# Kernel optimization log

Measured on AMD Instinct MI355X. Metric: run time of the kernel, lower is better.

The kernel has to match this reference:

```python
import jax, jax.numpy as jnp
import numpy as np

B, S, D = 8, 4096, 192
MEM_READ, MEM_WRITE, MEM_READY = 156, 157, 158


def setup_inputs() -> dict:
    key = jax.random.key(0)
    ks = jax.random.split(key, 9)
    inp = {"x": jax.random.normal(ks[0], (B, S, D), dtype=jnp.float32)}
    names = ["Wq_r", "Wk_r", "Wv_r", "Wo_r", "Wq_w", "Wk_w", "Wv_w", "Wo_w"]
    for i, n in enumerate(names):
        inp[n] = jax.random.normal(ks[i + 1], (D, D), dtype=jnp.float32) * 0.02
    return inp


def _attention(x, Wq, Wk, Wv, Wo):
    # single-head, non-causal PureAttention: q/k/v = x @ W.T, softmax(qk^T/sqrt(D)) v, then W_o
    q = jnp.einsum('bsd,ed->bse', x, Wq)
    k = jnp.einsum('bsd,ed->bse', x, Wk)
    v = jnp.einsum('bsd,ed->bse', x, Wv)
    scale = jnp.asarray(1.0 / np.sqrt(D), x.dtype)
    scores = jnp.einsum('bqe,bke->bqk', q, k) * scale  # [B,S,S]
    attn = jax.nn.softmax(scores, axis=-1)
    o = jnp.einsum('bqk,bke->bqe', attn, v)
    return jnp.einsum('bse,oe->bso', o, Wo)


def reference(x, Wq_r, Wk_r, Wv_r, Wo_r, Wq_w, Wk_w, Wv_w, Wo_w):
    read_flag = x[:, 0, MEM_READ]    # [B]
    write_flag = x[:, 0, MEM_WRITE]  # [B]
    read_res = _attention(x, Wq_r, Wk_r, Wv_r, Wo_r)
    write_res = _attention(x, Wq_w, Wk_w, Wv_w, Wo_w)
    rg = read_flag[:, None, None]
    wg = write_flag[:, None, None]
    out = x + rg * (read_res - x) + wg * (write_res - x)
    out = out.at[:, :, MEM_READ].set(0.0)
    out = out.at[:, :, MEM_WRITE].set(0.0)
    ready = (read_flag + write_flag)[:, None]  # broadcast over seq
    out = out.at[:, :, MEM_READY].set(jnp.broadcast_to(ready, out.shape[:2]))
    return out
```

## Files before the change

### kernel.cpp

```cpp
#include <hip/hip_runtime.h>
#include <stdint.h>

#define B_ 8
#define S_ 4096
#define D_ 192
#define M_ (B_*S_)

typedef short v8s __attribute__((ext_vector_type(8)));
typedef float v4f __attribute__((ext_vector_type(4)));
typedef unsigned short v4us __attribute__((ext_vector_type(4)));
typedef unsigned long long ull;

static __device__ __forceinline__ unsigned short f2bf(float f){
  union{float f; unsigned u;} v; v.f=f;
  unsigned u = v.u;
  unsigned r = (u + 0x7fffu + ((u>>16)&1u))>>16;
  return (unsigned short)r;
}
static __device__ __forceinline__ float fexp2(float x){
  return __builtin_amdgcn_exp2f(x);
}
static __device__ __forceinline__ unsigned cvtpk(float lo, float hi){
  unsigned r;
  asm("v_cvt_pk_bf16_f32 %0, %1, %2" : "=v"(r) : "v"(lo), "v"(hi));
  return r;
}

static __device__ __forceinline__ unsigned sw_fp8(float x){
  union{float f; unsigned u;} v; v.f = x;
  unsigned s = (v.u >> 24) & 0x80u;
  float a = fabsf(x);
  if (a < 0.001953125f) return s;
  if (a >= 240.f) return s | 0x7Eu;
  if (a < 0.015625f) {
    int m = (int)(a*512.f + 0.5f); if(m>7) m=7;
    return s | (unsigned)m;
  }
  int e = (int)((v.u >> 23) & 0xff) - 127;
  unsigned mant = (v.u >> 20) & 0x7u;
  unsigned rest = v.u & 0xFFFFFu;
  if (rest > 0x80000u || (rest == 0x80000u && (mant&1u))) mant++;
  unsigned ee = (unsigned)(e + 7);
  if (mant == 8u){ mant = 0u; ee++; }
  return s | (ee<<3) | mant;
}
template<bool HI>
static __device__ __forceinline__ unsigned pk8(float a, float b, unsigned old){
#if __has_builtin(__builtin_amdgcn_cvt_pk_fp8_f32)
  return __builtin_amdgcn_cvt_pk_fp8_f32(a, b, old, HI);
#else
  unsigned p = sw_fp8(a) | (sw_fp8(b)<<8);
  return HI ? ((old & 0x0000FFFFu) | (p<<16)) : ((old & 0xFFFF0000u) | p);
#endif
}

typedef const __attribute__((address_space(1))) unsigned int gu32;
typedef __attribute__((address_space(3))) unsigned int lu32;
#define GLL16(gp, lp) __builtin_amdgcn_global_load_lds((gu32*)(gp), (lu32*)(lp), 16, 0, 0)

__global__ void cvt_w_kernel(const float* w0,const float* w1,const float* w2,const float* w3,
                             const float* w4,const float* w5,const float* w6,const float* w7,
                             unsigned short* dst){
  int w = blockIdx.y;
  const float* src;
  switch(w){
    case 0: src=w0; break; case 1: src=w1; break; case 2: src=w2; break; case 3: src=w3; break;
    case 4: src=w4; break; case 5: src=w5; break; case 6: src=w6; break; default: src=w7; break;
  }
  int i = blockIdx.x*256 + threadIdx.x;
  float v = src[i];
  if(w==0 || w==4 || w==1 || w==5) v *= 0.32267249f;
  dst[(size_t)w*36864 + i] = f2bf(v);
}

__global__ __launch_bounds__(256) void proj_kernel(
    const float* __restrict__ x, const unsigned short* __restrict__ Wb,
    unsigned char* __restrict__ QK8, unsigned short* __restrict__ V16)
{
  __shared__ __align__(16) unsigned short Vstage[192*72];
  const size_t MDB = (size_t)M_*D_;
  const size_t MD  = (size_t)M_*D_;
  int path = blockIdx.y;
  int tid = threadIdx.x;
  int wid = tid>>6, lane = tid&63;
  int lr = lane&15, lg = lane>>4, kb = lg*8;
  int m0 = blockIdx.x*64 + wid*16;
  int row = m0 + lr;

  v8s a[6];
  #pragma unroll
  for(int c=0;c<6;c++){
    const float* xp = &x[(size_t)row*D_ + c*32 + kb];
    float4 f0 = *(const float4*)xp;
    float4 f1 = *(const float4*)(xp+4);
    v8s t;
    t[0]=(short)f2bf(f0.x); t[1]=(short)f2bf(f0.y); t[2]=(short)f2bf(f0.z); t[3]=(short)f2bf(f0.w);
    t[4]=(short)f2bf(f1.x); t[5]=(short)f2bf(f1.y); t[6]=(short)f2bf(f1.z); t[7]=(short)f2bf(f1.w);
    a[c]=t;
  }
  int bidx = m0 / S_;
  int sb   = (blockIdx.x*64) % S_;
  int sloc = wid*16 + lg*4;

  unsigned char* dstQ8 = QK8 + (size_t)path*2*MDB;
  for(int which=0; which<2; which++){
    const unsigned short* W = Wb + (size_t)(path*4 + which)*36864;
    unsigned char* dst = which==0 ? dstQ8 : dstQ8 + MDB;
    #pragma unroll
    for(int nt=0; nt<12; nt++){
      v4f acc = {0.f,0.f,0.f,0.f};
      int n = nt*16 + lr;
      #pragma unroll
      for(int c=0;c<6;c++){
        v8s bfr = *(const v8s*)&W[(size_t)n*D_ + c*32 + kb];
        acc = __builtin_amdgcn_mfma_f32_16x16x32_bf16(a[c], bfr, acc, 0,0,0);
      }
      int col = nt*16 + lr;
      int r0 = m0 + lg*4;
      #pragma unroll
      for(int r=0;r<4;r++){
        unsigned p = pk8<false>(acc[r], 0.f, 0u);
        dst[(size_t)(r0+r)*D_ + col] = (unsigned char)(p & 0xFF);
      }
    }
  }
  {
    const unsigned short* W = Wb + (size_t)(path*4 + 2)*36864;
    #pragma unroll
    for(int nt=0; nt<12; nt++){
      v4f acc = {0.f,0.f,0.f,0.f};
      int n = nt*16 + lr;
      #pragma unroll
      for(int c=0;c<6;c++){
        v8s bfr = *(const v8s*)&W[(size_t)n*D_ + c*32 + kb];
        acc = __builtin_amdgcn_mfma_f32_16x16x32_bf16(a[c], bfr, acc, 0,0,0);
      }
      int col = nt*16 + lr;
      v4us pk;
      pk[0]=f2bf(acc[0]); pk[1]=f2bf(acc[1]); pk[2]=f2bf(acc[2]); pk[3]=f2bf(acc[3]);
      *(v4us*)&Vstage[col*72 + sloc] = pk;
    }
    __syncthreads();
    unsigned short* dstV = V16 + (size_t)path*MD;
    size_t vg = (size_t)bidx*D_*S_ + sb;
    #pragma unroll
    for(int j=0;j<6;j++){
      int i = tid + j*256;
      int d = i>>3, s8 = (i&7)*8;
      *(v8s*)&dstV[vg + (size_t)d*S_ + s8] = *(const v8s*)&Vstage[d*72 + s8];
    }
  }
}

#define KSTR8 200

__global__ __launch_bounds__(512,4) void attn_kernel(
    const unsigned char* __restrict__ QK8,
    const unsigned short* __restrict__ V16,
    unsigned short* __restrict__ Ob)
{
  __shared__ __align__(16) unsigned char  KL[2][32*KSTR8];
  __shared__ __align__(16) unsigned short VL[3][192*32];

  int flat = blockIdx.x + 32*blockIdx.y + 256*blockIdx.z;
  int w = (flat&7)*64 + (flat>>3);
  int qi = w & 31;
  int b  = (w>>5) & 7;
  int z  = w>>8;

  const size_t MDB = (size_t)M_*D_;
  const unsigned char* Q8 = QK8 + (size_t)z*2*MDB;
  const unsigned char* K8 = Q8 + MDB;
  const unsigned short* Vt = V16 + (size_t)z*MDB;
  unsigned short* O = Ob + (size_t)z*MDB;

  int q0 = qi*128;
  int tid = threadIdx.x, wid=tid>>6, lane=tid&63;
  int lr = lane&15, lg = lane>>4;
  size_t bK = (size_t)b*S_*D_;
  size_t bV = (size_t)b*D_*S_;
  int qrow0 = q0 + wid*16;

  bool isK = wid < 4;
  int kt256 = tid & 255;
  int ksR = kt256>>3, ksC = (kt256&7)*24;
  int kLds = ksR*KSTR8 + ksC;
  int voff[3], vLds[3];
  #pragma unroll
  for(int j=0;j<3;j++){
    int i = (tid & 255) + j*256;
    int vrow = i>>2, vin = (i&3)*16;
    voff[j] = vrow*4096 + ((vin ^ (((vrow>>1)&3)<<4))>>1);
    vLds[j] = i*16;
  }
  int vro = ((lg*16) ^ (((lr>>1)&3)<<4)) >> 1;

  long qf8[6];
  {
    const unsigned char* qp = Q8 + bK + (size_t)(qrow0 + lr)*D_;
    #pragma unroll
    for(int c=0;c<6;c++) qf8[c] = *(const long*)(qp + c*32 + lg*8);
  }
  float lsum = 0.f;
  v4f oacc[12];
  #pragma unroll
  for(int e=0;e<12;e++) oacc[e] = (v4f){0.f,0.f,0.f,0.f};

  ull k0, k1, k2;
  auto kissue = [&](int t){
    if(isK){
      const unsigned char* kg = K8 + bK + (size_t)t*6144 + ksR*192 + ksC;
      k0 = *(const ull*)(kg);
      k1 = *(const ull*)(kg+8);
      k2 = *(const ull*)(kg+16);
    }
  };
  auto kwrite = [&](int buf){
    if(isK){
      unsigned char* d = &KL[buf][kLds];
      *(ull*)(d)    = k0;
      *(ull*)(d+8)  = k1;
      *(ull*)(d+16) = k2;
    }
  };
  auto vissue = [&](int t, int buf){
    if(!isK){
      const unsigned short* vg = Vt + bV + (size_t)t*32;
      #pragma unroll
      for(int j=0;j<3;j++) GLL16(vg + voff[j], ((unsigned char*)&VL[buf][0]) + vLds[j]);
    }
  };
  auto do_qk = [&](int kcur, v4f sacc[2]){
    __builtin_amdgcn_s_setprio(1);
    #pragma unroll
    for(int ct=0; ct<2; ct++){
      v4f s = {0.f,0.f,0.f,0.f};
      const unsigned char* rb = &KL[kcur][(ct*16+lr)*KSTR8];
      #pragma unroll
      for(int c=0;c<6;c++){
        long kf8 = *(const long*)(rb + c*32 + lg*8);
        s = __builtin_amdgcn_mfma_f32_16x16x32_fp8_fp8(kf8, qf8[c], s, 0,0,0);
      }
      sacc[ct]=s;
    }
    __builtin_amdgcn_s_setprio(0);
  };
  auto do_softmax = [&](v4f sacc[2], v8s& pa){
    float p00=fexp2(sacc[0][0]), p01=fexp2(sacc[0][1]);
    float p02=fexp2(sacc[0][2]), p03=fexp2(sacc[0][3]);
    float p10=fexp2(sacc[1][0]), p11=fexp2(sacc[1][1]);
    float p12=fexp2(sacc[1][2]), p13=fexp2(sacc[1][3]);
    lsum += ((p00+p01)+(p02+p03)) + ((p10+p11)+(p12+p13));
    unsigned X0=cvtpk(p00,p01), X1=cvtpk(p02,p03);
    unsigned Y0=cvtpk(p10,p11), Y1=cvtpk(p12,p13);
    asm("v_permlane32_swap_b32 %0, %1" : "+v"(Y0), "+v"(X0));
    asm("v_permlane32_swap_b32 %0, %1" : "+v"(Y1), "+v"(X1));
    asm("v_permlane16_swap_b32 %0, %1" : "+v"(Y0), "+v"(X0));
    asm("v_permlane16_swap_b32 %0, %1" : "+v"(Y1), "+v"(X1));
    union{ v8s s; unsigned w[4]; } u;
    u.w[0] = X0;  u.w[1] = X1;  u.w[2] = Y0;  u.w[3] = Y1;
    pa = u.s;
  };
  auto do_pv = [&](int vcur, v8s pa){
    __builtin_amdgcn_s_setprio(1);
    #pragma unroll
    for(int e=0;e<12;e++){
      v8s vbf = *(const v8s*)&VL[vcur][(e*16+lr)*32 + vro];
      oacc[e] = __builtin_amdgcn_mfma_f32_16x16x32_bf16(pa, vbf, oacc[e], 0,0,0);
    }
    __builtin_amdgcn_s_setprio(0);
  };

  kissue(0);
  vissue(0, 0);
  kwrite(0);
  asm volatile("s_waitcnt vmcnt(0)" ::: "memory");
  __syncthreads();

  v8s pa_prev;
  {
    v4f sacc[2];
    do_qk(0, sacc);
    kissue(1);
    vissue(1, 1);
    __builtin_amdgcn_sched_barrier(0);
    do_softmax(sacc, pa_prev);
    kwrite(1);
    asm volatile("s_waitcnt vmcnt(0)" ::: "memory");
    __syncthreads();
  }

  for(int t=1; t<128; t++){
    v4f sacc[2];
    do_qk(t&1, sacc);
    if(t<127){ kissue(t+1); vissue(t+1, (t+1)%3); }
    __builtin_amdgcn_sched_barrier(0);
    do_pv((t-1)%3, pa_prev);
    do_softmax(sacc, pa_prev);
    if(t<127) kwrite((t+1)&1);
    asm volatile("s_waitcnt vmcnt(0)" ::: "memory");
    __syncthreads();
  }
  do_pv(127%3, pa_prev);

  float ps = lsum;
  ps += __shfl_xor(ps, 16);
  ps += __shfl_xor(ps, 32);
  float iv = 1.0f/ps;
  float invr[4];
  #pragma unroll
  for(int r=0;r<4;r++) invr[r] = __shfl(iv, lg*4+r, 16);
  size_t orow0 = ((size_t)b*S_ + qrow0 + lg*4)*D_;
  #pragma unroll
  for(int e=0;e<12;e++){
    #pragma unroll
    for(int r=0;r<4;r++){
      O[orow0 + (size_t)r*D_ + e*16 + lr] = f2bf(oacc[e][r]*invr[r]);
    }
  }
}

__global__ __launch_bounds__(256) void final_kernel(
  const float* __restrict__ x,
  const unsigned short* __restrict__ Or,
  const unsigned short* __restrict__ Ow,
  const unsigned short* __restrict__ WoR,
  const unsigned short* __restrict__ WoW,
  float* __restrict__ out)
{
  int halfn = blockIdx.y;
  int tid=threadIdx.x, wid=tid>>6, lane=tid&63;
  int lr=lane&15, lg=lane>>4, kb=lg*8;
  int m0 = blockIdx.x*64 + wid*16;
  int arow = m0 + lr;
  v8s ar[6], aw[6];
  #pragma unroll
  for(int c=0;c<6;c++){
    ar[c] = *(const v8s*)&Or[(size_t)arow*D_ + c*32 + kb];
    aw[c] = *(const v8s*)&Ow[(size_t)arow*D_ + c*32 + kb];
  }
  int bidx = m0 / S_;
  float rf = x[(size_t)bidx*S_*D_ + 156];
  float wf = x[(size_t)bidx*S_*D_ + 157];
  #pragma unroll
  for(int ntl=0; ntl<6; ntl++){
    int nt = halfn*6 + ntl;
    v4f accR={0.f,0.f,0.f,0.f}, accW={0.f,0.f,0.f,0.f};
    int n = nt*16 + lr;
    #pragma unroll
    for(int c=0;c<6;c++){
      v8s br = *(const v8s*)&WoR[(size_t)n*D_ + c*32 + kb];
      accR = __builtin_amdgcn_mfma_f32_16x16x32_bf16(ar[c], br, accR,0,0,0);
      v8s bw = *(const v8s*)&WoW[(size_t)n*D_ + c*32 + kb];
      accW = __builtin_amdgcn_mfma_f32_16x16x32_bf16(aw[c], bw, accW,0,0,0);
    }
    #pragma unroll
    for(int r=0;r<4;r++){
      int row = m0 + lg*4 + r;
      int col = nt*16 + lr;
      float xv = x[(size_t)row*D_ + col];
      float val = xv + rf*(accR[r]-xv) + wf*(accW[r]-xv);
      if(col==156||col==157) val = 0.f;
      else if(col==158) val = rf+wf;
      out[(size_t)row*D_ + col] = val;
    }
  }
}

extern "C" void kernel_launch(void* const* d_in, const int* in_sizes, int n_in,
                              void* d_out, int out_size, void* d_ws, size_t ws_size,
                              hipStream_t stream) {
  const float* x = (const float*)d_in[0];
  char* wsb = (char*)d_ws;
  const size_t WSZ = 36864;
  const size_t MDB = (size_t)M_*D_;
  unsigned short* Wb  = (unsigned short*)wsb;
  unsigned char*  QK8 = (unsigned char*)(wsb + 8*WSZ*2);
  unsigned short* V16 = (unsigned short*)(wsb + 8*WSZ*2 + 4*MDB);
  unsigned short* Ob  = V16 + 2*MDB;

  cvt_w_kernel<<<dim3(144,8),256,0,stream>>>(
      (const float*)d_in[1],(const float*)d_in[2],(const float*)d_in[3],(const float*)d_in[4],
      (const float*)d_in[5],(const float*)d_in[6],(const float*)d_in[7],(const float*)d_in[8], Wb);

  proj_kernel<<<dim3(512,2),256,0,stream>>>(x, Wb, QK8, V16);
  attn_kernel<<<dim3(32,8,2),512,0,stream>>>(QK8, V16, Ob);
  final_kernel<<<dim3(512,2),256,0,stream>>>(x, Ob, Ob + MDB,
                                             Wb+3*WSZ, Wb+7*WSZ, (float*)d_out);
}
```

Baseline: 320.5 us.

## Split attention key range into two halves and merge partials in final kernel

Each attention block now covers half of the key sequence, so the grid doubles to 1024 blocks. Each block writes unnormalized bf16 outputs plus per-row softmax sums, and the final kernel adds the two partials and normalizes them before the output projection. The cross-iteration software pipeline, where PV of the previous tile overlapped QK of the current one, is replaced by a sequential QK-softmax-PV loop, and V buffering drops from three to two. The aim is better CU occupancy, at the cost of extra workspace traffic for the partials and less instruction-level overlap inside each block.

```diff
diff --git a/kernel.cpp b/kernel.cpp
--- a/kernel.cpp
+++ b/kernel.cpp
@@ -16,6 +16,9 @@
   unsigned u = v.u;
   unsigned r = (u + 0x7fffu + ((u>>16)&1u))>>16;
   return (unsigned short)r;
+}
+static __device__ __forceinline__ float bf2f(short s){
+  union{unsigned u; float f;} v; v.u = ((unsigned)(unsigned short)s)<<16; return v.f;
 }
 static __device__ __forceinline__ float fexp2(float x){
   return __builtin_amdgcn_exp2f(x);
@@ -157,22 +160,25 @@
 __global__ __launch_bounds__(512,4) void attn_kernel(
     const unsigned char* __restrict__ QK8,
     const unsigned short* __restrict__ V16,
-    unsigned short* __restrict__ Ob)
+    unsigned short* __restrict__ Ob,
+    float* __restrict__ Ls)
 {
   __shared__ __align__(16) unsigned char  KL[2][32*KSTR8];
-  __shared__ __align__(16) unsigned short VL[3][192*32];
-
-  int flat = blockIdx.x + 32*blockIdx.y + 256*blockIdx.z;
-  int w = (flat&7)*64 + (flat>>3);
-  int qi = w & 31;
-  int b  = (w>>5) & 7;
-  int z  = w>>8;
+  __shared__ __align__(16) unsigned short VL[2][192*32];
+
+  int flat = blockIdx.x + 64*blockIdx.y + 512*blockIdx.z;
+  int w = (flat&7)*128 + (flat>>3);
+  int qi   =  w       & 31;
+  int b    = (w>>5)   & 7;
+  int z    = (w>>8)   & 1;
+  int half = (w>>9)   & 1;
 
   const size_t MDB = (size_t)M_*D_;
   const unsigned char* Q8 = QK8 + (size_t)z*2*MDB;
   const unsigned char* K8 = Q8 + MDB;
   const unsigned short* Vt = V16 + (size_t)z*MDB;
-  unsigned short* O = Ob + (size_t)z*MDB;
+  unsigned short* O = Ob + (size_t)(z*2+half)*MDB;
+  float* Lp = Ls + (size_t)(z*2+half)*M_;
 
   int q0 = qi*128;
   int tid = threadIdx.x, wid=tid>>6, lane=tid&63;
@@ -271,74 +277,83 @@
     __builtin_amdgcn_s_setprio(0);
   };
 
-  kissue(0);
-  vissue(0, 0);
+  int t0 = half*64;
+  kissue(t0);
+  vissue(t0, 0);
   kwrite(0);
   asm volatile("s_waitcnt vmcnt(0)" ::: "memory");
   __syncthreads();
 
-  v8s pa_prev;
-  {
+  for(int tt=0; tt<64; tt++){
+    int t = t0 + tt;
+    int cur = tt&1;
+    if(tt<63){ kissue(t+1); vissue(t+1, cur^1); }
+    __builtin_amdgcn_sched_barrier(0);
+
     v4f sacc[2];
-    do_qk(0, sacc);
-    kissue(1);
-    vissue(1, 1);
-    __builtin_amdgcn_sched_barrier(0);
-    do_softmax(sacc, pa_prev);
-    kwrite(1);
+    do_qk(cur, sacc);
+    v8s pa;
+    do_softmax(sacc, pa);
+    do_pv(cur, pa);
+
+    if(tt<63) kwrite(cur^1);
     asm volatile("s_waitcnt vmcnt(0)" ::: "memory");
     __syncthreads();
   }
-
-  for(int t=1; t<128; t++){
-    v4f sacc[2];
-    do_qk(t&1, sacc);
-    if(t<127){ kissue(t+1); vissue(t+1, (t+1)%3); }
-    __builtin_amdgcn_sched_barrier(0);
-    do_pv((t-1)%3, pa_prev);
-    do_softmax(sacc, pa_prev);
-    if(t<127) kwrite((t+1)&1);
-    asm volatile("s_waitcnt vmcnt(0)" ::: "memory");
-    __syncthreads();
-  }
-  do_pv(127%3, pa_prev);
 
   float ps = lsum;
   ps += __shfl_xor(ps, 16);
   ps += __shfl_xor(ps, 32);
-  float iv = 1.0f/ps;
-  float invr[4];
-  #pragma unroll
-  for(int r=0;r<4;r++) invr[r] = __shfl(iv, lg*4+r, 16);
+  if(lane < 16){
+    Lp[(size_t)b*S_ + qrow0 + lr] = ps;
+  }
   size_t orow0 = ((size_t)b*S_ + qrow0 + lg*4)*D_;
   #pragma unroll
   for(int e=0;e<12;e++){
     #pragma unroll
     for(int r=0;r<4;r++){
-      O[orow0 + (size_t)r*D_ + e*16 + lr] = f2bf(oacc[e][r]*invr[r]);
+      O[orow0 + (size_t)r*D_ + e*16 + lr] = f2bf(oacc[e][r]);
     }
   }
 }
 
 __global__ __launch_bounds__(256) void final_kernel(
   const float* __restrict__ x,
-  const unsigned short* __restrict__ Or,
-  const unsigned short* __restrict__ Ow,
+  const unsigned short* __restrict__ Ob,
+  const float* __restrict__ Ls,
   const unsigned short* __restrict__ WoR,
   const unsigned short* __restrict__ WoW,
   float* __restrict__ out)
 {
+  const size_t MD = (size_t)M_*D_;
   int halfn = blockIdx.y;
   int tid=threadIdx.x, wid=tid>>6, lane=tid&63;
   int lr=lane&15, lg=lane>>4, kb=lg*8;
   int m0 = blockIdx.x*64 + wid*16;
   int arow = m0 + lr;
+
   v8s ar[6], aw[6];
   #pragma unroll
-  for(int c=0;c<6;c++){
-    ar[c] = *(const v8s*)&Or[(size_t)arow*D_ + c*32 + kb];
-    aw[c] = *(const v8s*)&Ow[(size_t)arow*D_ + c*32 + kb];
-  }
+  for(int path=0; path<2; path++){
+    const unsigned short* O0 = Ob + (size_t)path*2*MD;
+    const unsigned short* O1 = O0 + MD;
+    const float* L0 = Ls + (size_t)path*2*M_;
+    const float* L1 = L0 + M_;
+    float inv = 1.0f/(L0[arow] + L1[arow]);
+    #pragma unroll
+    for(int c=0;c<6;c++){
+      v8s x0 = *(const v8s*)&O0[(size_t)arow*D_ + c*32 + kb];
+      v8s x1 = *(const v8s*)&O1[(size_t)arow*D_ + c*32 + kb];
+      v8s t;
+      #pragma unroll
+      for(int j=0;j<8;j++){
+        float f = (bf2f(x0[j]) + bf2f(x1[j])) * inv;
+        t[j] = (short)f2bf(f);
+      }
+      if(path==0) ar[c]=t; else aw[c]=t;
+    }
+  }
+
   int bidx = m0 / S_;
   float rf = x[(size_t)bidx*S_*D_ + 156];
   float wf = x[(size_t)bidx*S_*D_ + 157];
@@ -378,13 +393,14 @@
   unsigned char*  QK8 = (unsigned char*)(wsb + 8*WSZ*2);
   unsigned short* V16 = (unsigned short*)(wsb + 8*WSZ*2 + 4*MDB);
   unsigned short* Ob  = V16 + 2*MDB;
+  float*          Ls  = (float*)(Ob + 4*MDB);
 
   cvt_w_kernel<<<dim3(144,8),256,0,stream>>>(
       (const float*)d_in[1],(const float*)d_in[2],(const float*)d_in[3],(const float*)d_in[4],
       (const float*)d_in[5],(const float*)d_in[6],(const float*)d_in[7],(const float*)d_in[8], Wb);
 
   proj_kernel<<<dim3(512,2),256,0,stream>>>(x, Wb, QK8, V16);
-  attn_kernel<<<dim3(32,8,2),512,0,stream>>>(QK8, V16, Ob);
-  final_kernel<<<dim3(512,2),256,0,stream>>>(x, Ob, Ob + MDB,
+  attn_kernel<<<dim3(64,8,2),512,0,stream>>>(QK8, V16, Ob, Ls);
+  final_kernel<<<dim3(512,2),256,0,stream>>>(x, Ob, Ls,
                                              Wb+3*WSZ, Wb+7*WSZ, (float*)d_out);
 }
```

Measured after the change: 327.1 us. 1.02x slower.

## Fuse output projection Wo into attention epilogue, simplify final combine

Applied to the files above, without the earlier changes.

Moves the Wo output projection into the attention kernel's epilogue. The PV MFMA operands are swapped so the O accumulator comes out transposed, then it is repacked through permlane swaps into an A operand for an MFMA against Wo read directly from global memory. The final kernel becomes a pure elementwise gated combine of x with the two projected results. This drops the separate GEMM pass and the re-read of the O tiles in the final stage, at the cost of more registers and uncached Wo loads in the attention epilogue.

```diff
diff --git a/kernel.cpp b/kernel.cpp
--- a/kernel.cpp
+++ b/kernel.cpp
@@ -16,6 +16,9 @@
   unsigned u = v.u;
   unsigned r = (u + 0x7fffu + ((u>>16)&1u))>>16;
   return (unsigned short)r;
+}
+static __device__ __forceinline__ float bf2f(unsigned short s){
+  union{unsigned u; float f;} v; v.u = ((unsigned)s)<<16; return v.f;
 }
 static __device__ __forceinline__ float fexp2(float x){
   return __builtin_amdgcn_exp2f(x);
@@ -157,7 +160,8 @@
 __global__ __launch_bounds__(512,4) void attn_kernel(
     const unsigned char* __restrict__ QK8,
     const unsigned short* __restrict__ V16,
-    unsigned short* __restrict__ Ob)
+    const unsigned short* __restrict__ Wb,
+    unsigned short* __restrict__ Rb)
 {
   __shared__ __align__(16) unsigned char  KL[2][32*KSTR8];
   __shared__ __align__(16) unsigned short VL[3][192*32];
@@ -172,7 +176,7 @@
   const unsigned char* Q8 = QK8 + (size_t)z*2*MDB;
   const unsigned char* K8 = Q8 + MDB;
   const unsigned short* Vt = V16 + (size_t)z*MDB;
-  unsigned short* O = Ob + (size_t)z*MDB;
+  unsigned short* R = Rb + (size_t)z*MDB;
 
   int q0 = qi*128;
   int tid = threadIdx.x, wid=tid>>6, lane=tid&63;
@@ -266,7 +270,7 @@
     #pragma unroll
     for(int e=0;e<12;e++){
       v8s vbf = *(const v8s*)&VL[vcur][(e*16+lr)*32 + vro];
-      oacc[e] = __builtin_amdgcn_mfma_f32_16x16x32_bf16(pa, vbf, oacc[e], 0,0,0);
+      oacc[e] = __builtin_amdgcn_mfma_f32_16x16x32_bf16(vbf, pa, oacc[e], 0,0,0);
     }
     __builtin_amdgcn_s_setprio(0);
   };
@@ -307,63 +311,69 @@
   ps += __shfl_xor(ps, 16);
   ps += __shfl_xor(ps, 32);
   float iv = 1.0f/ps;
-  float invr[4];
-  #pragma unroll
-  for(int r=0;r<4;r++) invr[r] = __shfl(iv, lg*4+r, 16);
-  size_t orow0 = ((size_t)b*S_ + qrow0 + lg*4)*D_;
-  #pragma unroll
-  for(int e=0;e<12;e++){
+
+  v8s oT[6];
+  #pragma unroll
+  for(int c=0;c<6;c++){
+    v4f lo = oacc[2*c], hi = oacc[2*c+1];
+    unsigned X0=cvtpk(lo[0]*iv, lo[1]*iv), X1=cvtpk(lo[2]*iv, lo[3]*iv);
+    unsigned Y0=cvtpk(hi[0]*iv, hi[1]*iv), Y1=cvtpk(hi[2]*iv, hi[3]*iv);
+    asm("v_permlane32_swap_b32 %0, %1" : "+v"(Y0), "+v"(X0));
+    asm("v_permlane32_swap_b32 %0, %1" : "+v"(Y1), "+v"(X1));
+    asm("v_permlane16_swap_b32 %0, %1" : "+v"(Y0), "+v"(X0));
+    asm("v_permlane16_swap_b32 %0, %1" : "+v"(Y1), "+v"(X1));
+    union{ v8s s; unsigned w[4]; } u;
+    u.w[0] = X0;  u.w[1] = X1;  u.w[2] = Y0;  u.w[3] = Y1;
+    oT[c] = u.s;
+  }
+  const unsigned short* Wo = Wb + (size_t)(z*4+3)*36864;
+  size_t rrow0 = ((size_t)b*S_ + qrow0 + lg*4)*D_;
+  #pragma unroll
+  for(int nt=0; nt<12; nt++){
+    v4f acc = {0.f,0.f,0.f,0.f};
+    int n = nt*16 + lr;
+    #pragma unroll
+    for(int c=0;c<6;c++){
+      v8s bw = *(const v8s*)&Wo[(size_t)n*D_ + c*32 + lg*8];
+      acc = __builtin_amdgcn_mfma_f32_16x16x32_bf16(oT[c], bw, acc, 0,0,0);
+    }
     #pragma unroll
     for(int r=0;r<4;r++){
-      O[orow0 + (size_t)r*D_ + e*16 + lr] = f2bf(oacc[e][r]*invr[r]);
+      R[rrow0 + (size_t)r*D_ + nt*16 + lr] = f2bf(acc[r]);
     }
   }
 }
 
 __global__ __launch_bounds__(256) void final_kernel(
   const float* __restrict__ x,
-  const unsigned short* __restrict__ Or,
-  const unsigned short* __restrict__ Ow,
-  const unsigned short* __restrict__ WoR,
-  const unsigned short* __restrict__ WoW,
+  const unsigned short* __restrict__ Rr,
+  const unsigned short* __restrict__ Rw,
   float* __restrict__ out)
 {
-  int halfn = blockIdx.y;
-  int tid=threadIdx.x, wid=tid>>6, lane=tid&63;
-  int lr=lane&15, lg=lane>>4, kb=lg*8;
-  int m0 = blockIdx.x*64 + wid*16;
-  int arow = m0 + lr;
-  v8s ar[6], aw[6];
-  #pragma unroll
-  for(int c=0;c<6;c++){
-    ar[c] = *(const v8s*)&Or[(size_t)arow*D_ + c*32 + kb];
-    aw[c] = *(const v8s*)&Ow[(size_t)arow*D_ + c*32 + kb];
-  }
-  int bidx = m0 / S_;
-  float rf = x[(size_t)bidx*S_*D_ + 156];
-  float wf = x[(size_t)bidx*S_*D_ + 157];
-  #pragma unroll
-  for(int ntl=0; ntl<6; ntl++){
-    int nt = halfn*6 + ntl;
-    v4f accR={0.f,0.f,0.f,0.f}, accW={0.f,0.f,0.f,0.f};
-    int n = nt*16 + lr;
-    #pragma unroll
-    for(int c=0;c<6;c++){
-      v8s br = *(const v8s*)&WoR[(size_t)n*D_ + c*32 + kb];
-      accR = __builtin_amdgcn_mfma_f32_16x16x32_bf16(ar[c], br, accR,0,0,0);
-      v8s bw = *(const v8s*)&WoW[(size_t)n*D_ + c*32 + kb];
-      accW = __builtin_amdgcn_mfma_f32_16x16x32_bf16(aw[c], bw, accW,0,0,0);
-    }
-    #pragma unroll
-    for(int r=0;r<4;r++){
-      int row = m0 + lg*4 + r;
-      int col = nt*16 + lr;
-      float xv = x[(size_t)row*D_ + col];
-      float val = xv + rf*(accR[r]-xv) + wf*(accW[r]-xv);
-      if(col==156||col==157) val = 0.f;
-      else if(col==158) val = rf+wf;
-      out[(size_t)row*D_ + col] = val;
-    }
+  const int NG = M_*D_/4;
+  int gid = blockIdx.x*256 + threadIdx.x;
+  for(int g = gid; g < NG; g += 2048*256){
+    int e0 = g*4;
+    int row = e0 / D_;
+    int col = e0 % D_;
+    int b = row >> 12;
+    size_t xb = (size_t)b*S_*D_;
+    float rf = x[xb + 156];
+    float wf = x[xb + 157];
+    float4 xv = *(const float4*)&x[e0];
+    v4us r4 = *(const v4us*)&Rr[e0];
+    v4us w4 = *(const v4us*)&Rw[e0];
+    float o[4];
+    #pragma unroll
+    for(int j=0;j<4;j++){
+      float xvj = (&xv.x)[j];
+      float val = xvj + rf*(bf2f(r4[j]) - xvj) + wf*(bf2f(w4[j]) - xvj);
+      int cj = col + j;
+      if(cj==156||cj==157) val = 0.f;
+      else if(cj==158) val = rf+wf;
+      o[j] = val;
+    }
+    *(float4*)&out[e0] = *(float4*)o;
   }
 }
 
@@ -377,14 +387,13 @@
   unsigned short* Wb  = (unsigned short*)wsb;
   unsigned char*  QK8 = (unsigned char*)(wsb + 8*WSZ*2);
   unsigned short* V16 = (unsigned short*)(wsb + 8*WSZ*2 + 4*MDB);
-  unsigned short* Ob  = V16 + 2*MDB;
+  unsigned short* Rb  = V16 + 2*MDB;
 
   cvt_w_kernel<<<dim3(144,8),256,0,stream>>>(
       (const float*)d_in[1],(const float*)d_in[2],(const float*)d_in[3],(const float*)d_in[4],
       (const float*)d_in[5],(const float*)d_in[6],(const float*)d_in[7],(const float*)d_in[8], Wb);
 
   proj_kernel<<<dim3(512,2),256,0,stream>>>(x, Wb, QK8, V16);
-  attn_kernel<<<dim3(32,8,2),512,0,stream>>>(QK8, V16, Ob);
-  final_kernel<<<dim3(512,2),256,0,stream>>>(x, Ob, Ob + MDB,
-                                             Wb+3*WSZ, Wb+7*WSZ, (float*)d_out);
-}
+  attn_kernel<<<dim3(32,8,2),512,0,stream>>>(QK8, V16, Wb, Rb);
+  final_kernel<<<2048,256,0,stream>>>(x, Rb, Rb + MDB, (float*)d_out);
+}
```

Measured after the change: 322.5 us. About the same (+0.6%).

## Quantize V and P to FP8 and use fp8 MFMA for PV

Applied to the files above, without the earlier changes.

V is now stored as FP8 in a pre-tiled per-32-key layout (192 rows with stride 40 bytes), and the softmax probabilities are converted to FP8 so the P·V product uses the fp8 MFMA instead of bf16. This halves V global and LDS traffic, removes the swizzled address computation, and uses the higher-throughput fp8 matrix instruction. The cost is extra bf16-to-fp8 conversion work in the softmax step and lower precision for P and V, which could hurt accuracy.

```diff
diff --git a/kernel.cpp b/kernel.cpp
--- a/kernel.cpp
+++ b/kernel.cpp
@@ -5,6 +5,7 @@
 #define S_ 4096
 #define D_ 192
 #define M_ (B_*S_)
+#define VTILE 7680
 
 typedef short v8s __attribute__((ext_vector_type(8)));
 typedef float v4f __attribute__((ext_vector_type(4)));
@@ -24,6 +25,9 @@
   unsigned r;
   asm("v_cvt_pk_bf16_f32 %0, %1, %2" : "=v"(r) : "v"(lo), "v"(hi));
   return r;
+}
+static __device__ __forceinline__ float asf(unsigned u){
+  union{unsigned u; float f;} v; v.u=u; return v.f;
 }
 
 static __device__ __forceinline__ unsigned sw_fp8(float x){
@@ -75,11 +79,10 @@
 
 __global__ __launch_bounds__(256) void proj_kernel(
     const float* __restrict__ x, const unsigned short* __restrict__ Wb,
-    unsigned char* __restrict__ QK8, unsigned short* __restrict__ V16)
+    unsigned char* __restrict__ QK8, unsigned char* __restrict__ V8)
 {
-  __shared__ __align__(16) unsigned short Vstage[192*72];
+  __shared__ __align__(16) unsigned char Vstage8[2*VTILE];
   const size_t MDB = (size_t)M_*D_;
-  const size_t MD  = (size_t)M_*D_;
   int path = blockIdx.y;
   int tid = threadIdx.x;
   int wid = tid>>6, lane = tid&63;
@@ -126,6 +129,7 @@
   }
   {
     const unsigned short* W = Wb + (size_t)(path*4 + 2)*36864;
+    int t2 = sloc >> 5, s32 = sloc & 31;
     #pragma unroll
     for(int nt=0; nt<12; nt++){
       v4f acc = {0.f,0.f,0.f,0.f};
@@ -136,18 +140,17 @@
         acc = __builtin_amdgcn_mfma_f32_16x16x32_bf16(a[c], bfr, acc, 0,0,0);
       }
       int col = nt*16 + lr;
-      v4us pk;
-      pk[0]=f2bf(acc[0]); pk[1]=f2bf(acc[1]); pk[2]=f2bf(acc[2]); pk[3]=f2bf(acc[3]);
-      *(v4us*)&Vstage[col*72 + sloc] = pk;
+      unsigned pk4 = pk8<false>(acc[0], acc[1], 0u);
+      pk4 = pk8<true>(acc[2], acc[3], pk4);
+      *(unsigned*)&Vstage8[t2*VTILE + col*40 + s32] = pk4;
     }
     __syncthreads();
-    unsigned short* dstV = V16 + (size_t)path*MD;
-    size_t vg = (size_t)bidx*D_*S_ + sb;
-    #pragma unroll
-    for(int j=0;j<6;j++){
+    unsigned char* dstV = V8 + (size_t)path*((size_t)B_*128*VTILE)
+                        + ((size_t)bidx*128 + (sb>>5))*VTILE;
+    #pragma unroll
+    for(int j=0;j<4;j++){
       int i = tid + j*256;
-      int d = i>>3, s8 = (i&7)*8;
-      *(v8s*)&dstV[vg + (size_t)d*S_ + s8] = *(const v8s*)&Vstage[d*72 + s8];
+      if(i<960) *(v8s*)&dstV[i*16] = *(const v8s*)&Vstage8[i*16];
     }
   }
 }
@@ -156,11 +159,11 @@
 
 __global__ __launch_bounds__(512,4) void attn_kernel(
     const unsigned char* __restrict__ QK8,
-    const unsigned short* __restrict__ V16,
+    const unsigned char* __restrict__ V8,
     unsigned short* __restrict__ Ob)
 {
-  __shared__ __align__(16) unsigned char  KL[2][32*KSTR8];
-  __shared__ __align__(16) unsigned short VL[3][192*32];
+  __shared__ __align__(16) unsigned char KL[2][32*KSTR8];
+  __shared__ __align__(16) unsigned char VL8[3][VTILE];
 
   int flat = blockIdx.x + 32*blockIdx.y + 256*blockIdx.z;
   int w = (flat&7)*64 + (flat>>3);
@@ -171,29 +174,19 @@
   const size_t MDB = (size_t)M_*D_;
   const unsigned char* Q8 = QK8 + (size_t)z*2*MDB;
   const unsigned char* K8 = Q8 + MDB;
-  const unsigned short* Vt = V16 + (size_t)z*MDB;
+  const unsigned char* Vp = V8 + (size_t)z*((size_t)B_*128*VTILE);
   unsigned short* O = Ob + (size_t)z*MDB;
 
   int q0 = qi*128;
   int tid = threadIdx.x, wid=tid>>6, lane=tid&63;
   int lr = lane&15, lg = lane>>4;
   size_t bK = (size_t)b*S_*D_;
-  size_t bV = (size_t)b*D_*S_;
   int qrow0 = q0 + wid*16;
 
   bool isK = wid < 4;
   int kt256 = tid & 255;
   int ksR = kt256>>3, ksC = (kt256&7)*24;
   int kLds = ksR*KSTR8 + ksC;
-  int voff[3], vLds[3];
-  #pragma unroll
-  for(int j=0;j<3;j++){
-    int i = (tid & 255) + j*256;
-    int vrow = i>>2, vin = (i&3)*16;
-    voff[j] = vrow*4096 + ((vin ^ (((vrow>>1)&3)<<4))>>1);
-    vLds[j] = i*16;
-  }
-  int vro = ((lg*16) ^ (((lr>>1)&3)<<4)) >> 1;
 
   long qf8[6];
   {
@@ -225,9 +218,12 @@
   };
   auto vissue = [&](int t, int buf){
     if(!isK){
-      const unsigned short* vg = Vt + bV + (size_t)t*32;
-      #pragma unroll
-      for(int j=0;j<3;j++) GLL16(vg + voff[j], ((unsigned char*)&VL[buf][0]) + vLds[j]);
+      const unsigned char* vg = Vp + ((size_t)b*128 + t)*VTILE;
+      #pragma unroll
+      for(int j=0;j<2;j++){
+        int i = (tid&255) + j*256;
+        if(i<480) GLL16(vg + i*16, &VL8[buf][i*16]);
+      }
     }
   };
   auto do_qk = [&](int kcur, v4f sacc[2]){
@@ -245,7 +241,7 @@
     }
     __builtin_amdgcn_s_setprio(0);
   };
-  auto do_softmax = [&](v4f sacc[2], v8s& pa){
+  auto do_softmax = [&](v4f sacc[2], long& pa8){
     float p00=fexp2(sacc[0][0]), p01=fexp2(sacc[0][1]);
     float p02=fexp2(sacc[0][2]), p03=fexp2(sacc[0][3]);
     float p10=fexp2(sacc[1][0]), p11=fexp2(sacc[1][1]);
@@ -257,16 +253,20 @@
     asm("v_permlane32_swap_b32 %0, %1" : "+v"(Y1), "+v"(X1));
     asm("v_permlane16_swap_b32 %0, %1" : "+v"(Y0), "+v"(X0));
     asm("v_permlane16_swap_b32 %0, %1" : "+v"(Y1), "+v"(X1));
-    union{ v8s s; unsigned w[4]; } u;
-    u.w[0] = X0;  u.w[1] = X1;  u.w[2] = Y0;  u.w[3] = Y1;
-    pa = u.s;
-  };
-  auto do_pv = [&](int vcur, v8s pa){
+    float e0 = asf(X0<<16), e1 = asf(X0 & 0xffff0000u);
+    float e2 = asf(X1<<16), e3 = asf(X1 & 0xffff0000u);
+    float e4 = asf(Y0<<16), e5 = asf(Y0 & 0xffff0000u);
+    float e6 = asf(Y1<<16), e7 = asf(Y1 & 0xffff0000u);
+    unsigned lo = pk8<false>(e0,e1,0u); lo = pk8<true>(e2,e3,lo);
+    unsigned hi = pk8<false>(e4,e5,0u); hi = pk8<true>(e6,e7,hi);
+    pa8 = (long)(((ull)hi<<32) | (ull)lo);
+  };
+  auto do_pv = [&](int vcur, long pa8){
     __builtin_amdgcn_s_setprio(1);
     #pragma unroll
     for(int e=0;e<12;e++){
-      v8s vbf = *(const v8s*)&VL[vcur][(e*16+lr)*32 + vro];
-      oacc[e] = __builtin_amdgcn_mfma_f32_16x16x32_bf16(pa, vbf, oacc[e], 0,0,0);
+      long vb8 = *(const long*)&VL8[vcur][(e*16+lr)*40 + lg*8];
+      oacc[e] = __builtin_amdgcn_mfma_f32_16x16x32_fp8_fp8(pa8, vb8, oacc[e], 0,0,0);
     }
     __builtin_amdgcn_s_setprio(0);
   };
@@ -277,7 +277,7 @@
   asm volatile("s_waitcnt vmcnt(0)" ::: "memory");
   __syncthreads();
 
-  v8s pa_prev;
+  long pa_prev;
   {
     v4f sacc[2];
     do_qk(0, sacc);
@@ -374,17 +374,18 @@
   char* wsb = (char*)d_ws;
   const size_t WSZ = 36864;
   const size_t MDB = (size_t)M_*D_;
+  const size_t V8SZ = (size_t)2*B_*128*VTILE;
   unsigned short* Wb  = (unsigned short*)wsb;
   unsigned char*  QK8 = (unsigned char*)(wsb + 8*WSZ*2);
-  unsigned short* V16 = (unsigned short*)(wsb + 8*WSZ*2 + 4*MDB);
-  unsigned short* Ob  = V16 + 2*MDB;
+  unsigned char*  V8  = QK8 + 4*MDB;
+  unsigned short* Ob  = (unsigned short*)(V8 + V8SZ);
 
   cvt_w_kernel<<<dim3(144,8),256,0,stream>>>(
       (const float*)d_in[1],(const float*)d_in[2],(const float*)d_in[3],(const float*)d_in[4],
       (const float*)d_in[5],(const float*)d_in[6],(const float*)d_in[7],(const float*)d_in[8], Wb);
 
-  proj_kernel<<<dim3(512,2),256,0,stream>>>(x, Wb, QK8, V16);
-  attn_kernel<<<dim3(32,8,2),512,0,stream>>>(QK8, V16, Ob);
+  proj_kernel<<<dim3(512,2),256,0,stream>>>(x, Wb, QK8, V8);
+  attn_kernel<<<dim3(32,8,2),512,0,stream>>>(QK8, V8, Ob);
   final_kernel<<<dim3(512,2),256,0,stream>>>(x, Ob, Ob + MDB,
                                              Wb+3*WSZ, Wb+7*WSZ, (float*)d_out);
 }
```

After: 309.9 us. 1.03x faster.
